# Optimization experiments

Measured on AMD Instinct MI355X. Metric: run time of the kernel, lower is better.

The kernel has to match this reference:

```python
import jax, jax.numpy as jnp
import numpy as np

EPS = 1e-8  # torch F.cosine_similarity eps


def setup_inputs() -> dict:
    key = jax.random.key(0)
    ks = jax.random.split(key, 12)
    B, S, D, C, V = 2, 1024, 512, 1000, 50000
    sc = lambda fan_in: 1.0 / np.sqrt(fan_in)
    return {
        "spectrum_real": jax.random.normal(ks[0], (B, S, D), jnp.float32),
        "spectrum_imag": jax.random.normal(ks[1], (B, S, D), jnp.float32),
        "concept_spectra_real": jax.random.normal(ks[2], (C, D), jnp.float32),
        "concept_spectra_imag": jax.random.normal(ks[3], (C, D), jnp.float32),
        "W1": jax.random.normal(ks[4], (2 * D, D), jnp.float32) * sc(2 * D),
        "b1": jnp.zeros((D,), jnp.float32),
        "W2": jax.random.normal(ks[5], (D, 512), jnp.float32) * sc(D),
        "b2": jnp.zeros((512,), jnp.float32),
        "W3": jax.random.normal(ks[6], (512, 768), jnp.float32) * sc(512),
        "b3": jnp.zeros((768,), jnp.float32),
        "W4": jax.random.normal(ks[7], (768, V), jnp.float32) * sc(768),
        "b4": jnp.zeros((V,), jnp.float32),
        "top_k": 5,
    }


def reference(spectrum_real, spectrum_imag, concept_spectra_real, concept_spectra_imag,
              W1, b1, W2, b2, W3, b3, W4, b4, top_k):
    # --- find_spectral_matches: batched cosine similarity over magnitudes + top-k ---
    mag = jnp.sqrt(spectrum_real ** 2 + spectrum_imag ** 2)            # [B,S,D]
    cmag = jnp.sqrt(concept_spectra_real ** 2 + concept_spectra_imag ** 2)  # [C,D]
    # cosine sim = (x . y) / (max(||x||, eps) * max(||y||, eps))
    dots = jnp.einsum('bsd,cd->bsc', mag, cmag)                        # [B,S,C]
    xn = jnp.maximum(jnp.linalg.norm(mag, axis=-1), EPS)               # [B,S]
    yn = jnp.maximum(jnp.linalg.norm(cmag, axis=-1), EPS)              # [C]
    sims = dots / (xn[..., None] * yn[None, None, :])                  # [B,S,C]
    top_sims, top_idx = jax.lax.top_k(sims, top_k)                     # [B,S,k]

    # --- decode_spectral_concepts: cat(real, imag) -> MLP -> vocab logits ---
    gelu = lambda x: jax.nn.gelu(x, approximate=False)                 # torch nn.GELU default
    x = jnp.concatenate([spectrum_real, spectrum_imag], axis=-1)       # [B,S,2D]
    h = gelu(x @ W1 + b1)
    h = gelu(h @ W2 + b2)
    h = gelu(h @ W3 + b3)
    logits = h @ W4 + b4                                               # [B,S,V]
    return top_sims, top_idx, logits
```

## Files before the change

kernel.cpp:

```cpp
#include <hip/hip_runtime.h>
#include <hip/hip_bf16.h>
#include <hip/hip_fp8.h>

#define CEPS 1e-8f

typedef __attribute__((ext_vector_type(8))) __bf16 bf16x8;
typedef __attribute__((ext_vector_type(4))) float f32x4;

__device__ __forceinline__ void gload_lds16(const void* g, void* l) {
  __builtin_amdgcn_global_load_lds((const __attribute__((address_space(1))) unsigned int*)g,
                                   (__attribute__((address_space(3))) unsigned int*)l, 16, 0, 0);
}

__device__ __forceinline__ float gelu_f(float v) {
  return 0.5f * v * (1.0f + erff(v * 0.70710678118654752f));
}

__device__ __forceinline__ unsigned char f32_to_e4m3(float v) {
  __hip_fp8_e4m3 t(v);
  return (unsigned char)t.__x;
}

__global__ __launch_bounds__(256) void k_mag(const float* __restrict__ re, const float* __restrict__ im,
                                             float* __restrict__ mag, __hip_bfloat16* __restrict__ xcat,
                                             float* __restrict__ xn) {
  int row = blockIdx.x;
  const float* r = re + (size_t)row * 512;
  const float* q = im + (size_t)row * 512;
  double ss = 0.0;
  for (int d = threadIdx.x; d < 512; d += 256) {
    float a = r[d], b = q[d];
    float s = __fadd_rn(__fmul_rn(a, a), __fmul_rn(b, b));
    float m = __fsqrt_rn(s);
    mag[(size_t)row * 512 + d] = m;
    xcat[(size_t)row * 1024 + d] = __float2bfloat16(a);
    xcat[(size_t)row * 1024 + 512 + d] = __float2bfloat16(b);
    ss += (double)m * (double)m;
  }
  for (int off = 32; off; off >>= 1) ss += __shfl_xor(ss, off);
  __shared__ double red[4];
  int lane = threadIdx.x & 63, wave = threadIdx.x >> 6;
  if (lane == 0) red[wave] = ss;
  __syncthreads();
  if (threadIdx.x == 0) {
    double tot = red[0] + red[1] + red[2] + red[3];
    float n = (float)sqrt(tot);
    xn[row] = fmaxf(n, CEPS);
  }
}

__global__ __launch_bounds__(256) void k_cmag(const float* __restrict__ cre, const float* __restrict__ cim,
                                              float* __restrict__ cmagT, float* __restrict__ yn) {
  int c = blockIdx.x;
  const float* r = cre + (size_t)c * 512;
  const float* q = cim + (size_t)c * 512;
  double ss = 0.0;
  for (int d = threadIdx.x; d < 512; d += 256) {
    float a = r[d], b = q[d];
    float s = __fadd_rn(__fmul_rn(a, a), __fmul_rn(b, b));
    float m = __fsqrt_rn(s);
    cmagT[(size_t)d * 1000 + c] = m;
    ss += (double)m * (double)m;
  }
  for (int off = 32; off; off >>= 1) ss += __shfl_xor(ss, off);
  __shared__ double red[4];
  int lane = threadIdx.x & 63, wave = threadIdx.x >> 6;
  if (lane == 0) red[wave] = ss;
  __syncthreads();
  if (threadIdx.x == 0) {
    double tot = red[0] + red[1] + red[2] + red[3];
    float n = (float)sqrt(tot);
    yn[c] = fmaxf(n, CEPS);
  }
}

__global__ __launch_bounds__(256) void k_dots(const float* __restrict__ A, const float* __restrict__ Bm,
                                              float* __restrict__ Cm, int M, int N, int K, int ldc,
                                              const float* __restrict__ xn, const float* __restrict__ yn) {
  __shared__ double As[16][64];
  __shared__ double Bs[16][64];
  const int tid = threadIdx.x;
  const int m0 = blockIdx.y * 64, n0 = blockIdx.x * 64;
  const int tx = tid & 15, ty4 = tid >> 4;
  const int ar = tid >> 2, ak = (tid & 3) << 2;
  const int bk = tid >> 4, bn = (tid & 15) << 2;
  double acc[4][4] = {};
  for (int k0 = 0; k0 < K; k0 += 16) {
    float4 a4 = *(const float4*)(A + (size_t)(m0 + ar) * K + k0 + ak);
    As[ak + 0][ar] = (double)a4.x; As[ak + 1][ar] = (double)a4.y;
    As[ak + 2][ar] = (double)a4.z; As[ak + 3][ar] = (double)a4.w;
    float4 b4 = make_float4(0.f, 0.f, 0.f, 0.f);
    if (n0 + bn < N) b4 = *(const float4*)(Bm + (size_t)(k0 + bk) * N + n0 + bn);
    Bs[bk][bn + 0] = (double)b4.x; Bs[bk][bn + 1] = (double)b4.y;
    Bs[bk][bn + 2] = (double)b4.z; Bs[bk][bn + 3] = (double)b4.w;
    __syncthreads();
#pragma unroll
    for (int kk = 0; kk < 16; ++kk) {
      double av[4], bv[4];
#pragma unroll
      for (int i = 0; i < 4; ++i) av[i] = As[kk][ty4 + i * 16];
#pragma unroll
      for (int j = 0; j < 4; ++j) bv[j] = Bs[kk][tx + j * 16];
#pragma unroll
      for (int i = 0; i < 4; ++i)
#pragma unroll
        for (int j = 0; j < 4; ++j)
          acc[i][j] = fma(av[i], bv[j], acc[i][j]);
    }
    __syncthreads();
  }
#pragma unroll
  for (int i = 0; i < 4; ++i) {
    int row = m0 + ty4 + i * 16;
#pragma unroll
    for (int j = 0; j < 4; ++j) {
      int col = n0 + tx + j * 16;
      if (col >= N) continue;
      double d = acc[i][j] / ((double)xn[row] * (double)yn[col]);
      Cm[(size_t)row * ldc + col] = (float)d;
    }
  }
}

__global__ __launch_bounds__(256) void k_topk(const float* __restrict__ sims,
                                              float* __restrict__ top_sims, float* __restrict__ top_idx) {
  int lane = threadIdx.x & 63, wave = threadIdx.x >> 6;
  int row = blockIdx.x * 4 + wave;
  const float* s = sims + (size_t)row * 1000;
  float v[16];
  int idx[16];
#pragma unroll
  for (int t = 0; t < 16; ++t) {
    int c = lane + t * 64;
    if (c < 1000) { v[t] = s[c]; idx[t] = c; }
    else { v[t] = -1e30f; idx[t] = 1 << 20; }
  }
  for (int j = 0; j < 5; ++j) {
    float bv = -1e30f; int bi = 1 << 20;
#pragma unroll
    for (int t = 0; t < 16; ++t) {
      if (v[t] > bv || (v[t] == bv && idx[t] < bi)) { bv = v[t]; bi = idx[t]; }
    }
    float rv = bv; int ri = bi;
#pragma unroll
    for (int off = 32; off; off >>= 1) {
      float ov = __shfl_xor(rv, off);
      int oi = __shfl_xor(ri, off);
      if (ov > rv || (ov == rv && oi < ri)) { rv = ov; ri = oi; }
    }
    if (lane == 0) {
      top_sims[(size_t)row * 5 + j] = rv;
      top_idx[(size_t)row * 5 + j] = (float)ri;
    }
#pragma unroll
    for (int t = 0; t < 16; ++t)
      if (idx[t] == ri) v[t] = -1e30f;
  }
}

template <int OUTT>
__global__ __launch_bounds__(256) void k_tr(const float* __restrict__ W, void* __restrict__ Wt,
                                            int K, int N) {
  __shared__ float t32[64][65];
  int n0 = blockIdx.x * 64, k0 = blockIdx.y * 64;
  int tid = threadIdx.x;
  {
    int nc = tid & 15, kr4 = tid >> 4;
#pragma unroll
    for (int p = 0; p < 4; ++p) {
      int kr = p * 16 + kr4;
      int n = n0 + nc * 4;
      float4 v = make_float4(0.f, 0.f, 0.f, 0.f);
      if (n < N) v = *(const float4*)(W + (size_t)(k0 + kr) * N + n);
      t32[kr][nc * 4 + 0] = v.x; t32[kr][nc * 4 + 1] = v.y;
      t32[kr][nc * 4 + 2] = v.z; t32[kr][nc * 4 + 3] = v.w;
    }
  }
  __syncthreads();
  {
    int kc = tid & 15, nr4 = tid >> 4;
#pragma unroll
    for (int p = 0; p < 4; ++p) {
      int nr = p * 16 + nr4;
      if (OUTT == 0) {
        ushort4 o;
        __hip_bfloat16 h0 = __float2bfloat16(t32[kc * 4 + 0][nr]);
        __hip_bfloat16 h1 = __float2bfloat16(t32[kc * 4 + 1][nr]);
        __hip_bfloat16 h2 = __float2bfloat16(t32[kc * 4 + 2][nr]);
        __hip_bfloat16 h3 = __float2bfloat16(t32[kc * 4 + 3][nr]);
        o.x = *(unsigned short*)&h0; o.y = *(unsigned short*)&h1;
        o.z = *(unsigned short*)&h2; o.w = *(unsigned short*)&h3;
        *(ushort4*)((unsigned short*)Wt + (size_t)(n0 + nr) * K + k0 + kc * 4) = o;
      } else {
        unsigned int o = (unsigned int)f32_to_e4m3(t32[kc * 4 + 0][nr]) |
                         ((unsigned int)f32_to_e4m3(t32[kc * 4 + 1][nr]) << 8) |
                         ((unsigned int)f32_to_e4m3(t32[kc * 4 + 2][nr]) << 16) |
                         ((unsigned int)f32_to_e4m3(t32[kc * 4 + 3][nr]) << 24);
        *(unsigned int*)((unsigned char*)Wt + (size_t)(n0 + nr) * K + k0 + kc * 4) = o;
      }
    }
  }
}

template <int OUTT>
__global__ __launch_bounds__(256) void gemm_mfma_bt(const __hip_bfloat16* __restrict__ A,
                                                    const __hip_bfloat16* __restrict__ Bt,
                                                    void* __restrict__ C, int M, int N, int K,
                                                    int ldc, const float* __restrict__ bias) {
  __shared__ short Al[128 * 32];
  __shared__ short Bl[128 * 32];
  const int tid = threadIdx.x, lane = tid & 63, wave = tid >> 6;
  const int m0 = blockIdx.y * 128, n0 = blockIdx.x * 128;
  const int wr = wave >> 1, wc = wave & 1;
  f32x4 acc[4][4];
  f32x4 zero4 = {0.f, 0.f, 0.f, 0.f};
#pragma unroll
  for (int i = 0; i < 4; ++i)
#pragma unroll
    for (int j = 0; j < 4; ++j) acc[i][j] = zero4;

  const short* Ag = (const short*)A;
  const short* Bg = (const short*)Bt;
  for (int k0 = 0; k0 < K; k0 += 32) {
#pragma unroll
    for (int s = 0; s < 2; ++s) {
      int seg = wave + s * 4;
      int elem = seg * 512 + lane * 8;
      int row = elem >> 5, kk = elem & 31;
      gload_lds16(Ag + (size_t)(m0 + row) * K + k0 + kk, Al + elem);
      gload_lds16(Bg + (size_t)(n0 + row) * K + k0 + kk, Bl + elem);
    }
    __syncthreads();
    bf16x8 af[4], bfr[4];
    const int fr = lane & 15, fk = (lane >> 4) << 3;
#pragma unroll
    for (int i = 0; i < 4; ++i)
      af[i] = *(const bf16x8*)(Al + (wr * 64 + i * 16 + fr) * 32 + fk);
#pragma unroll
    for (int j = 0; j < 4; ++j)
      bfr[j] = *(const bf16x8*)(Bl + (wc * 64 + j * 16 + fr) * 32 + fk);
#pragma unroll
    for (int i = 0; i < 4; ++i)
#pragma unroll
      for (int j = 0; j < 4; ++j)
        acc[i][j] = __builtin_amdgcn_mfma_f32_16x16x32_bf16(af[i], bfr[j], acc[i][j], 0, 0, 0);
    __syncthreads();
  }
  const int fr = lane & 15, fq = lane >> 4;
#pragma unroll
  for (int j = 0; j < 4; ++j) {
    int col = n0 + wc * 64 + j * 16 + fr;
    if (col >= N) continue;
    float bv = bias[col];
#pragma unroll
    for (int i = 0; i < 4; ++i) {
      int rbase = m0 + wr * 64 + i * 16 + fq * 4;
#pragma unroll
      for (int r = 0; r < 4; ++r) {
        float v = gelu_f(acc[i][j][r] + bv);
        if (OUTT == 0)
          ((__hip_bfloat16*)C)[(size_t)(rbase + r) * ldc + col] = __float2bfloat16(v);
        else
          ((unsigned char*)C)[(size_t)(rbase + r) * ldc + col] = f32_to_e4m3(v);
      }
    }
  }
}

__global__ __launch_bounds__(256, 2) void gemm_v9(const unsigned char* __restrict__ A8,
                                                  const unsigned char* __restrict__ B8,
                                                  float* __restrict__ C,
                                                  const float* __restrict__ bias) {
  const int KNT = 12;
  const int Kd = 768, Nd = 50000, ldc = 50000;
  __shared__ unsigned char As[2][256 * 64];
  __shared__ unsigned char Bs[2][128 * 64];
  const int tid = threadIdx.x, lane = tid & 63, wave = tid >> 6;
  const int wm = wave >> 1, wn = wave & 1;

  const int xcd = blockIdx.x & 7, j = blockIdx.x >> 3;
  const int mt = j & 7;
  const int ntile = xcd + 8 * (j >> 3);
  const int m0 = mt * 256, n0 = ntile * 128;

  f32x4 acc[8][4];
  f32x4 z4 = {0.f, 0.f, 0.f, 0.f};
#pragma unroll
  for (int q = 0; q < 8; ++q)
#pragma unroll
    for (int p = 0; p < 4; ++p) acc[q][p] = z4;

  auto stageA = [&](int kt, int buf) {
    if (kt >= KNT) return;
    const int k0 = kt * 64;
#pragma unroll
    for (int r = 0; r < 4; ++r) {
      int idx = r * 256 + tid;
      int row = idx >> 2, c = idx & 3;
      int src = ((c * 2) ^ (row & 6)) * 8;
      gload_lds16(A8 + (size_t)(m0 + row) * Kd + k0 + src, &As[buf][row * 64 + c * 16]);
    }
  };
  auto stageB = [&](int kt, int buf) {
    if (kt >= KNT) return;
    const int k0 = kt * 64;
#pragma unroll
    for (int r = 0; r < 2; ++r) {
      int idx = r * 256 + tid;
      int row = idx >> 2, c = idx & 3;
      int src = ((c * 2) ^ (row & 6)) * 8;
      gload_lds16(B8 + (size_t)(n0 + row) * Kd + k0 + src, &Bs[buf][row * 64 + c * 16]);
    }
  };

  stageA(0, 0); stageB(0, 0);
  stageA(1, 1); stageB(1, 1);

  for (int g = 0; g < KNT; ++g) {
    const int buf = g & 1;
    if (g < KNT - 1) asm volatile("s_waitcnt vmcnt(6)" ::: "memory");
    else             asm volatile("s_waitcnt vmcnt(0)" ::: "memory");
    __builtin_amdgcn_sched_barrier(0);
    __builtin_amdgcn_s_barrier();
    __builtin_amdgcn_sched_barrier(0);

    long bfr[4][2];
#pragma unroll
    for (int p = 0; p < 4; ++p) {
      int row = wn * 64 + p * 16 + (lane & 15);
#pragma unroll
      for (int kh = 0; kh < 2; ++kh) {
        int slot = (kh * 4 + (lane >> 4)) ^ (row & 6);
        bfr[p][kh] = *(const long*)(&Bs[buf][row * 64 + slot * 8]);
      }
    }
#pragma unroll
    for (int q = 0; q < 8; ++q) {
      int rowA = wm * 128 + q * 16 + (lane & 15);
      long af[2];
#pragma unroll
      for (int kh = 0; kh < 2; ++kh) {
        int slot = (kh * 4 + (lane >> 4)) ^ (rowA & 6);
        af[kh] = *(const long*)(&As[buf][rowA * 64 + slot * 8]);
      }
#pragma unroll
      for (int kh = 0; kh < 2; ++kh)
#pragma unroll
        for (int p = 0; p < 4; ++p)
          acc[q][p] = __builtin_amdgcn_mfma_f32_16x16x32_fp8_fp8(bfr[p][kh], af[kh], acc[q][p], 0, 0, 0);
    }

    __builtin_amdgcn_sched_barrier(0);
    __builtin_amdgcn_s_barrier();
    __builtin_amdgcn_sched_barrier(0);
    stageA(g + 2, buf);
    stageB(g + 2, buf);
  }

  const int colq = (lane >> 4) * 4;
  float4 bias4[4];
#pragma unroll
  for (int p = 0; p < 4; ++p) {
    int colbase = n0 + wn * 64 + p * 16 + colq;
    bias4[p] = (colbase < Nd) ? *(const float4*)(bias + colbase) : make_float4(0.f, 0.f, 0.f, 0.f);
  }
#pragma unroll
  for (int q = 0; q < 8; ++q) {
    int row = m0 + wm * 128 + q * 16 + (lane & 15);
#pragma unroll
    for (int p = 0; p < 4; ++p) {
      int colbase = n0 + wn * 64 + p * 16 + colq;
      if (colbase < Nd) {
        f32x4 v = acc[q][p];
        float4 o = make_float4(v[0] + bias4[p].x, v[1] + bias4[p].y,
                               v[2] + bias4[p].z, v[3] + bias4[p].w);
        *(float4*)(&C[(size_t)row * ldc + colbase]) = o;
      }
    }
  }
}

extern "C" void kernel_launch(void* const* d_in, const int* in_sizes, int n_in,
                              void* d_out, int out_size, void* d_ws, size_t ws_size,
                              hipStream_t stream) {
  const float* sre = (const float*)d_in[0];
  const float* simg = (const float*)d_in[1];
  const float* cre = (const float*)d_in[2];
  const float* cim = (const float*)d_in[3];
  const float* W1 = (const float*)d_in[4];
  const float* b1 = (const float*)d_in[5];
  const float* W2 = (const float*)d_in[6];
  const float* b2 = (const float*)d_in[7];
  const float* W3 = (const float*)d_in[8];
  const float* b3 = (const float*)d_in[9];
  const float* W4 = (const float*)d_in[10];
  const float* b4 = (const float*)d_in[11];

  const int M = 2048, D = 512, Cc = 1000, V = 50000, K1 = 1024, H3 = 768;
  const int Npad2 = 392 * 128;

  char* ws = (char*)d_ws;
  size_t off = 0;
  auto alloc = [&](size_t bytes) {
    char* p = ws + off;
    off = (off + bytes + 255) & ~(size_t)255;
    return p;
  };
  __hip_bfloat16* xcatb = (__hip_bfloat16*)alloc((size_t)M * K1 * 2);
  float* mag = (float*)alloc((size_t)M * D * 4);
  float* cmagT = (float*)alloc((size_t)D * Cc * 4);
  float* xn = (float*)alloc((size_t)M * 4);
  float* yn = (float*)alloc((size_t)Cc * 4);
  float* simsb = (float*)alloc((size_t)M * Cc * 4);
  __hip_bfloat16* h1b = (__hip_bfloat16*)alloc((size_t)M * 512 * 2);
  __hip_bfloat16* h2b = (__hip_bfloat16*)alloc((size_t)M * 512 * 2);
  unsigned char* h3f8 = (unsigned char*)alloc((size_t)M * H3);
  __hip_bfloat16* w1t = (__hip_bfloat16*)alloc((size_t)512 * K1 * 2);
  __hip_bfloat16* w2t = (__hip_bfloat16*)alloc((size_t)512 * 512 * 2);
  __hip_bfloat16* w3t = (__hip_bfloat16*)alloc((size_t)H3 * 512 * 2);
  unsigned char* w4f8 = (unsigned char*)alloc((size_t)Npad2 * H3);

  float* top_sims = (float*)d_out;
  float* top_idx = (float*)d_out + (size_t)M * 5;
  float* logits = (float*)d_out + (size_t)M * 5 * 2;

  k_tr<0><<<dim3(512 / 64, K1 / 64), dim3(256), 0, stream>>>(W1, (void*)w1t, K1, 512);
  k_tr<0><<<dim3(512 / 64, 512 / 64), dim3(256), 0, stream>>>(W2, (void*)w2t, 512, 512);
  k_tr<0><<<dim3(H3 / 64, 512 / 64), dim3(256), 0, stream>>>(W3, (void*)w3t, 512, H3);
  k_tr<1><<<dim3(Npad2 / 64, H3 / 64), dim3(256), 0, stream>>>(W4, (void*)w4f8, H3, V);

  k_cmag<<<dim3(Cc), dim3(256), 0, stream>>>(cre, cim, cmagT, yn);
  k_mag<<<dim3(M), dim3(256), 0, stream>>>(sre, simg, mag, xcatb, xn);
  k_dots<<<dim3((Cc + 63) / 64, M / 64), dim3(256), 0, stream>>>(mag, cmagT, simsb, M, Cc, D, Cc, xn, yn);
  k_topk<<<dim3(M / 4), dim3(256), 0, stream>>>(simsb, top_sims, top_idx);

  gemm_mfma_bt<0><<<dim3(512 / 128, M / 128), dim3(256), 0, stream>>>(xcatb, w1t, (void*)h1b, M, 512, K1, 512, b1);
  gemm_mfma_bt<0><<<dim3(512 / 128, M / 128), dim3(256), 0, stream>>>(h1b, w2t, (void*)h2b, M, 512, 512, 512, b2);
  gemm_mfma_bt<1><<<dim3(H3 / 128, M / 128), dim3(256), 0, stream>>>(h2b, w3t, (void*)h3f8, M, H3, 512, H3, b3);

  gemm_v9<<<dim3(8 * 392), dim3(256), 0, stream>>>(h3f8, w4f8, logits, b4);
}
```

Before: 475.2 us.

## Merge independent stages into fused multi-role kernels to overlap work

Combines the weight transposes, concept-magnitude and spectrum-magnitude kernels into one launch (k_pre). It also runs the W4 fp8 transpose alongside the first MLP layer, and interleaves the fp64 cosine-dot tiles among the fp8 vocab GEMM blocks in a single launch that shares LDS through a union. This cuts the launch count from 12 to 6 and lets small, underutilizing stages fill idle CUs while large ones run. It also adds s_setprio around the MFMA section of the vocab GEMM. In exchange, block-index dispatch logic adds branching, and the fp64 dots tiles may run unevenly against the GEMM tiles.

New measurement: 407.2 us. 14.3% less time.

```diff
diff --git a/kernel.cpp b/kernel.cpp
--- a/kernel.cpp
+++ b/kernel.cpp
@@ -21,10 +21,11 @@
   return (unsigned char)t.__x;
 }
 
-__global__ __launch_bounds__(256) void k_mag(const float* __restrict__ re, const float* __restrict__ im,
-                                             float* __restrict__ mag, __hip_bfloat16* __restrict__ xcat,
-                                             float* __restrict__ xn) {
-  int row = blockIdx.x;
+
+__device__ __forceinline__ void dev_mag(double* red, const float* __restrict__ re,
+                                        const float* __restrict__ im, float* __restrict__ mag,
+                                        __hip_bfloat16* __restrict__ xcat, float* __restrict__ xn,
+                                        int row) {
   const float* r = re + (size_t)row * 512;
   const float* q = im + (size_t)row * 512;
   double ss = 0.0;
@@ -38,7 +39,6 @@
     ss += (double)m * (double)m;
   }
   for (int off = 32; off; off >>= 1) ss += __shfl_xor(ss, off);
-  __shared__ double red[4];
   int lane = threadIdx.x & 63, wave = threadIdx.x >> 6;
   if (lane == 0) red[wave] = ss;
   __syncthreads();
@@ -49,9 +49,9 @@
   }
 }
 
-__global__ __launch_bounds__(256) void k_cmag(const float* __restrict__ cre, const float* __restrict__ cim,
-                                              float* __restrict__ cmagT, float* __restrict__ yn) {
-  int c = blockIdx.x;
+__device__ __forceinline__ void dev_cmag(double* red, const float* __restrict__ cre,
+                                         const float* __restrict__ cim, float* __restrict__ cmagT,
+                                         float* __restrict__ yn, int c) {
   const float* r = cre + (size_t)c * 512;
   const float* q = cim + (size_t)c * 512;
   double ss = 0.0;
@@ -63,7 +63,6 @@
     ss += (double)m * (double)m;
   }
   for (int off = 32; off; off >>= 1) ss += __shfl_xor(ss, off);
-  __shared__ double red[4];
   int lane = threadIdx.x & 63, wave = threadIdx.x >> 6;
   if (lane == 0) red[wave] = ss;
   __syncthreads();
@@ -74,95 +73,10 @@
   }
 }
 
-__global__ __launch_bounds__(256) void k_dots(const float* __restrict__ A, const float* __restrict__ Bm,
-                                              float* __restrict__ Cm, int M, int N, int K, int ldc,
-                                              const float* __restrict__ xn, const float* __restrict__ yn) {
-  __shared__ double As[16][64];
-  __shared__ double Bs[16][64];
-  const int tid = threadIdx.x;
-  const int m0 = blockIdx.y * 64, n0 = blockIdx.x * 64;
-  const int tx = tid & 15, ty4 = tid >> 4;
-  const int ar = tid >> 2, ak = (tid & 3) << 2;
-  const int bk = tid >> 4, bn = (tid & 15) << 2;
-  double acc[4][4] = {};
-  for (int k0 = 0; k0 < K; k0 += 16) {
-    float4 a4 = *(const float4*)(A + (size_t)(m0 + ar) * K + k0 + ak);
-    As[ak + 0][ar] = (double)a4.x; As[ak + 1][ar] = (double)a4.y;
-    As[ak + 2][ar] = (double)a4.z; As[ak + 3][ar] = (double)a4.w;
-    float4 b4 = make_float4(0.f, 0.f, 0.f, 0.f);
-    if (n0 + bn < N) b4 = *(const float4*)(Bm + (size_t)(k0 + bk) * N + n0 + bn);
-    Bs[bk][bn + 0] = (double)b4.x; Bs[bk][bn + 1] = (double)b4.y;
-    Bs[bk][bn + 2] = (double)b4.z; Bs[bk][bn + 3] = (double)b4.w;
-    __syncthreads();
-#pragma unroll
-    for (int kk = 0; kk < 16; ++kk) {
-      double av[4], bv[4];
-#pragma unroll
-      for (int i = 0; i < 4; ++i) av[i] = As[kk][ty4 + i * 16];
-#pragma unroll
-      for (int j = 0; j < 4; ++j) bv[j] = Bs[kk][tx + j * 16];
-#pragma unroll
-      for (int i = 0; i < 4; ++i)
-#pragma unroll
-        for (int j = 0; j < 4; ++j)
-          acc[i][j] = fma(av[i], bv[j], acc[i][j]);
-    }
-    __syncthreads();
-  }
-#pragma unroll
-  for (int i = 0; i < 4; ++i) {
-    int row = m0 + ty4 + i * 16;
-#pragma unroll
-    for (int j = 0; j < 4; ++j) {
-      int col = n0 + tx + j * 16;
-      if (col >= N) continue;
-      double d = acc[i][j] / ((double)xn[row] * (double)yn[col]);
-      Cm[(size_t)row * ldc + col] = (float)d;
-    }
-  }
-}
-
-__global__ __launch_bounds__(256) void k_topk(const float* __restrict__ sims,
-                                              float* __restrict__ top_sims, float* __restrict__ top_idx) {
-  int lane = threadIdx.x & 63, wave = threadIdx.x >> 6;
-  int row = blockIdx.x * 4 + wave;
-  const float* s = sims + (size_t)row * 1000;
-  float v[16];
-  int idx[16];
-#pragma unroll
-  for (int t = 0; t < 16; ++t) {
-    int c = lane + t * 64;
-    if (c < 1000) { v[t] = s[c]; idx[t] = c; }
-    else { v[t] = -1e30f; idx[t] = 1 << 20; }
-  }
-  for (int j = 0; j < 5; ++j) {
-    float bv = -1e30f; int bi = 1 << 20;
-#pragma unroll
-    for (int t = 0; t < 16; ++t) {
-      if (v[t] > bv || (v[t] == bv && idx[t] < bi)) { bv = v[t]; bi = idx[t]; }
-    }
-    float rv = bv; int ri = bi;
-#pragma unroll
-    for (int off = 32; off; off >>= 1) {
-      float ov = __shfl_xor(rv, off);
-      int oi = __shfl_xor(ri, off);
-      if (ov > rv || (ov == rv && oi < ri)) { rv = ov; ri = oi; }
-    }
-    if (lane == 0) {
-      top_sims[(size_t)row * 5 + j] = rv;
-      top_idx[(size_t)row * 5 + j] = (float)ri;
-    }
-#pragma unroll
-    for (int t = 0; t < 16; ++t)
-      if (idx[t] == ri) v[t] = -1e30f;
-  }
-}
-
 template <int OUTT>
-__global__ __launch_bounds__(256) void k_tr(const float* __restrict__ W, void* __restrict__ Wt,
-                                            int K, int N) {
-  __shared__ float t32[64][65];
-  int n0 = blockIdx.x * 64, k0 = blockIdx.y * 64;
+__device__ __forceinline__ void dev_tr(float (*t32)[65], const float* __restrict__ W,
+                                       void* __restrict__ Wt, int K, int N, int bx, int by) {
+  int n0 = bx * 64, k0 = by * 64;
   int tid = threadIdx.x;
   {
     int nc = tid & 15, kr4 = tid >> 4;
@@ -203,14 +117,12 @@
 }
 
 template <int OUTT>
-__global__ __launch_bounds__(256) void gemm_mfma_bt(const __hip_bfloat16* __restrict__ A,
-                                                    const __hip_bfloat16* __restrict__ Bt,
-                                                    void* __restrict__ C, int M, int N, int K,
-                                                    int ldc, const float* __restrict__ bias) {
-  __shared__ short Al[128 * 32];
-  __shared__ short Bl[128 * 32];
+__device__ __forceinline__ void dev_mlp(short* Al, short* Bl, const __hip_bfloat16* __restrict__ A,
+                                        const __hip_bfloat16* __restrict__ Bt, void* __restrict__ C,
+                                        int M, int N, int K, int ldc, const float* __restrict__ bias,
+                                        int bx, int by) {
   const int tid = threadIdx.x, lane = tid & 63, wave = tid >> 6;
-  const int m0 = blockIdx.y * 128, n0 = blockIdx.x * 128;
+  const int m0 = by * 128, n0 = bx * 128;
   const int wr = wave >> 1, wc = wave & 1;
   f32x4 acc[4][4];
   f32x4 zero4 = {0.f, 0.f, 0.f, 0.f};
@@ -267,18 +179,64 @@
   }
 }
 
-__global__ __launch_bounds__(256, 2) void gemm_v9(const unsigned char* __restrict__ A8,
-                                                  const unsigned char* __restrict__ B8,
-                                                  float* __restrict__ C,
-                                                  const float* __restrict__ bias) {
+__device__ __forceinline__ void dev_dots(double (*As)[64], double (*Bs)[64],
+                                         const float* __restrict__ A, const float* __restrict__ Bm,
+                                         float* __restrict__ Cm, int M, int N, int K, int ldc,
+                                         const float* __restrict__ xn, const float* __restrict__ yn,
+                                         int nb, int mb) {
+  const int tid = threadIdx.x;
+  const int m0 = mb * 64, n0 = nb * 64;
+  const int tx = tid & 15, ty4 = tid >> 4;
+  const int ar = tid >> 2, ak = (tid & 3) << 2;
+  const int bk = tid >> 4, bn = (tid & 15) << 2;
+  double acc[4][4] = {};
+  for (int k0 = 0; k0 < K; k0 += 16) {
+    float4 a4 = *(const float4*)(A + (size_t)(m0 + ar) * K + k0 + ak);
+    As[ak + 0][ar] = (double)a4.x; As[ak + 1][ar] = (double)a4.y;
+    As[ak + 2][ar] = (double)a4.z; As[ak + 3][ar] = (double)a4.w;
+    float4 b4 = make_float4(0.f, 0.f, 0.f, 0.f);
+    if (n0 + bn < N) b4 = *(const float4*)(Bm + (size_t)(k0 + bk) * N + n0 + bn);
+    Bs[bk][bn + 0] = (double)b4.x; Bs[bk][bn + 1] = (double)b4.y;
+    Bs[bk][bn + 2] = (double)b4.z; Bs[bk][bn + 3] = (double)b4.w;
+    __syncthreads();
+#pragma unroll
+    for (int kk = 0; kk < 16; ++kk) {
+      double av[4], bv[4];
+#pragma unroll
+      for (int i = 0; i < 4; ++i) av[i] = As[kk][ty4 + i * 16];
+#pragma unroll
+      for (int j = 0; j < 4; ++j) bv[j] = Bs[kk][tx + j * 16];
+#pragma unroll
+      for (int i = 0; i < 4; ++i)
+#pragma unroll
+        for (int j = 0; j < 4; ++j)
+          acc[i][j] = fma(av[i], bv[j], acc[i][j]);
+    }
+    __syncthreads();
+  }
+#pragma unroll
+  for (int i = 0; i < 4; ++i) {
+    int row = m0 + ty4 + i * 16;
+#pragma unroll
+    for (int j = 0; j < 4; ++j) {
+      int col = n0 + tx + j * 16;
+      if (col >= N) continue;
+      double d = acc[i][j] / ((double)xn[row] * (double)yn[col]);
+      Cm[(size_t)row * ldc + col] = (float)d;
+    }
+  }
+}
+
+__device__ __forceinline__ void dev_gemm(unsigned char (*As)[16384], unsigned char (*Bs)[8192],
+                                         const unsigned char* __restrict__ A8,
+                                         const unsigned char* __restrict__ B8,
+                                         float* __restrict__ C, const float* __restrict__ bias,
+                                         int xcd, int j) {
   const int KNT = 12;
   const int Kd = 768, Nd = 50000, ldc = 50000;
-  __shared__ unsigned char As[2][256 * 64];
-  __shared__ unsigned char Bs[2][128 * 64];
   const int tid = threadIdx.x, lane = tid & 63, wave = tid >> 6;
   const int wm = wave >> 1, wn = wave & 1;
 
-  const int xcd = blockIdx.x & 7, j = blockIdx.x >> 3;
   const int mt = j & 7;
   const int ntile = xcd + 8 * (j >> 3);
   const int m0 = mt * 256, n0 = ntile * 128;
@@ -334,6 +292,7 @@
         bfr[p][kh] = *(const long*)(&Bs[buf][row * 64 + slot * 8]);
       }
     }
+    __builtin_amdgcn_s_setprio(1);
 #pragma unroll
     for (int q = 0; q < 8; ++q) {
       int rowA = wm * 128 + q * 16 + (lane & 15);
@@ -349,6 +308,7 @@
         for (int p = 0; p < 4; ++p)
           acc[q][p] = __builtin_amdgcn_mfma_f32_16x16x32_fp8_fp8(bfr[p][kh], af[kh], acc[q][p], 0, 0, 0);
     }
+    __builtin_amdgcn_s_setprio(0);
 
     __builtin_amdgcn_sched_barrier(0);
     __builtin_amdgcn_s_barrier();
@@ -377,6 +337,119 @@
         *(float4*)(&C[(size_t)row * ldc + colbase]) = o;
       }
     }
+  }
+}
+
+
+__global__ __launch_bounds__(256) void k_pre(const float* W1, __hip_bfloat16* w1t,
+                                             const float* W2, __hip_bfloat16* w2t,
+                                             const float* W3, __hip_bfloat16* w3t,
+                                             const float* cre, const float* cim, float* cmagT, float* yn,
+                                             const float* sre, const float* simg, float* mag,
+                                             __hip_bfloat16* xcat, float* xn) {
+  __shared__ float t32[64][65];
+  __shared__ double red[4];
+  int bid = blockIdx.x;
+  if (bid < 128) {
+    dev_tr<0>(t32, W1, (void*)w1t, 1024, 512, bid & 7, bid >> 3);
+  } else if (bid < 192) {
+    int t = bid - 128;
+    dev_tr<0>(t32, W2, (void*)w2t, 512, 512, t & 7, t >> 3);
+  } else if (bid < 288) {
+    int t = bid - 192;
+    dev_tr<0>(t32, W3, (void*)w3t, 512, 768, t % 12, t / 12);
+  } else if (bid < 1288) {
+    dev_cmag(red, cre, cim, cmagT, yn, bid - 288);
+  } else {
+    dev_mag(red, sre, simg, mag, xcat, xn, bid - 1288);
+  }
+}
+
+__global__ __launch_bounds__(256) void k_l1w4(const __hip_bfloat16* xcat, const __hip_bfloat16* w1t,
+                                              __hip_bfloat16* h1b, const float* b1,
+                                              const float* W4, unsigned char* w4f8) {
+  __shared__ short Al[128 * 32];
+  __shared__ short Bl[128 * 32];
+  __shared__ float t32[64][65];
+  int bid = blockIdx.x;
+  if (bid < 64) {
+    dev_mlp<0>(Al, Bl, xcat, w1t, (void*)h1b, 2048, 512, 1024, 512, b1, bid & 3, bid >> 2);
+  } else {
+    int t = bid - 64;
+    dev_tr<1>(t32, W4, (void*)w4f8, 768, 50000, t % 784, t / 784);
+  }
+}
+
+template <int OUTT>
+__global__ __launch_bounds__(256) void k_mlp(const __hip_bfloat16* A, const __hip_bfloat16* Bt,
+                                             void* C, int M, int N, int K, int ldc, const float* bias) {
+  __shared__ short Al[128 * 32];
+  __shared__ short Bl[128 * 32];
+  dev_mlp<OUTT>(Al, Bl, A, Bt, C, M, N, K, ldc, bias, blockIdx.x, blockIdx.y);
+}
+
+union KMainSmem {
+  struct { unsigned char As[2][16384]; unsigned char Bs[2][8192]; } g;
+  struct { double As[16][64]; double Bs[16][64]; } d;
+};
+
+__global__ __launch_bounds__(256, 2) void k_main(const unsigned char* __restrict__ A8,
+                                                 const unsigned char* __restrict__ B8,
+                                                 float* __restrict__ C, const float* __restrict__ bias,
+                                                 const float* __restrict__ mag,
+                                                 const float* __restrict__ cmagT,
+                                                 float* __restrict__ simsb,
+                                                 const float* __restrict__ xn,
+                                                 const float* __restrict__ yn) {
+  __shared__ KMainSmem sm;
+  const int bid = blockIdx.x;
+  const int g = bid >> 3;
+  const bool isDots = ((g % 7) == 3) && (g <= 444);
+  if (isDots) {
+    int dgi = (g - 3) / 7;
+    int id = dgi * 8 + (bid & 7);
+    dev_dots(sm.d.As, sm.d.Bs, mag, cmagT, simsb, 2048, 1000, 512, 1000, xn, yn,
+             id & 15, id >> 4);
+  } else {
+    int dots_before = (g < 3) ? 0 : min(64, (g + 4) / 7);
+    int jg = g - dots_before;
+    dev_gemm(sm.g.As, sm.g.Bs, A8, B8, C, bias, bid & 7, jg);
+  }
+}
+
+__global__ __launch_bounds__(256) void k_topk(const float* __restrict__ sims,
+                                              float* __restrict__ top_sims, float* __restrict__ top_idx) {
+  int lane = threadIdx.x & 63, wave = threadIdx.x >> 6;
+  int row = blockIdx.x * 4 + wave;
+  const float* s = sims + (size_t)row * 1000;
+  float v[16];
+  int idx[16];
+#pragma unroll
+  for (int t = 0; t < 16; ++t) {
+    int c = lane + t * 64;
+    if (c < 1000) { v[t] = s[c]; idx[t] = c; }
+    else { v[t] = -1e30f; idx[t] = 1 << 20; }
+  }
+  for (int j = 0; j < 5; ++j) {
+    float bv = -1e30f; int bi = 1 << 20;
+#pragma unroll
+    for (int t = 0; t < 16; ++t) {
+      if (v[t] > bv || (v[t] == bv && idx[t] < bi)) { bv = v[t]; bi = idx[t]; }
+    }
+    float rv = bv; int ri = bi;
+#pragma unroll
+    for (int off = 32; off; off >>= 1) {
+      float ov = __shfl_xor(rv, off);
+      int oi = __shfl_xor(ri, off);
+      if (ov > rv || (ov == rv && oi < ri)) { rv = ov; ri = oi; }
+    }
+    if (lane == 0) {
+      top_sims[(size_t)row * 5 + j] = rv;
+      top_idx[(size_t)row * 5 + j] = (float)ri;
+    }
+#pragma unroll
+    for (int t = 0; t < 16; ++t)
+      if (idx[t] == ri) v[t] = -1e30f;
   }
 }
 
@@ -424,19 +497,11 @@
   float* top_idx = (float*)d_out + (size_t)M * 5;
   float* logits = (float*)d_out + (size_t)M * 5 * 2;
 
-  k_tr<0><<<dim3(512 / 64, K1 / 64), dim3(256), 0, stream>>>(W1, (void*)w1t, K1, 512);
-  k_tr<0><<<dim3(512 / 64, 512 / 64), dim3(256), 0, stream>>>(W2, (void*)w2t, 512, 512);
-  k_tr<0><<<dim3(H3 / 64, 512 / 64), dim3(256), 0, stream>>>(W3, (void*)w3t, 512, H3);
-  k_tr<1><<<dim3(Npad2 / 64, H3 / 64), dim3(256), 0, stream>>>(W4, (void*)w4f8, H3, V);
-
-  k_cmag<<<dim3(Cc), dim3(256), 0, stream>>>(cre, cim, cmagT, yn);
-  k_mag<<<dim3(M), dim3(256), 0, stream>>>(sre, simg, mag, xcatb, xn);
-  k_dots<<<dim3((Cc + 63) / 64, M / 64), dim3(256), 0, stream>>>(mag, cmagT, simsb, M, Cc, D, Cc, xn, yn);
+  k_pre<<<dim3(3336), dim3(256), 0, stream>>>(W1, w1t, W2, w2t, W3, w3t,
+                                              cre, cim, cmagT, yn, sre, simg, mag, xcatb, xn);
+  k_l1w4<<<dim3(64 + 9408), dim3(256), 0, stream>>>(xcatb, w1t, h1b, b1, W4, w4f8);
+  k_mlp<0><<<dim3(4, 16), dim3(256), 0, stream>>>(h1b, w2t, (void*)h2b, M, 512, 512, 512, b2);
+  k_mlp<1><<<dim3(6, 16), dim3(256), 0, stream>>>(h2b, w3t, (void*)h3f8, M, H3, 512, H3, b3);
+  k_main<<<dim3(3648), dim3(256), 0, stream>>>(h3f8, w4f8, logits, b4, mag, cmagT, simsb, xn, yn);
   k_topk<<<dim3(M / 4), dim3(256), 0, stream>>>(simsb, top_sims, top_idx);
-
-  gemm_mfma_bt<0><<<dim3(512 / 128, M / 128), dim3(256), 0, stream>>>(xcatb, w1t, (void*)h1b, M, 512, K1, 512, b1);
-  gemm_mfma_bt<0><<<dim3(512 / 128, M / 128), dim3(256), 0, stream>>>(h1b, w2t, (void*)h2b, M, 512, 512, 512, b2);
-  gemm_mfma_bt<1><<<dim3(H3 / 128, M / 128), dim3(256), 0, stream>>>(h2b, w3t, (void*)h3f8, M, H3, 512, H3, b3);
-
-  gemm_v9<<<dim3(8 * 392), dim3(256), 0, stream>>>(h3f8, w4f8, logits, b4);
-}
+}
```
